# Kernel optimization log

Hardware: AMD Instinct MI355X
Metric: run time of the kernel (lower is better)

## Reference

```python
import jax, jax.numpy as jnp
import numpy as np

N_FIELDS = 8
HIDDEN = 128
GEO = 15
APP = 32
N_PTS = 524288


def setup_inputs() -> dict:
    key = jax.random.key(0)
    ks = jax.random.split(key, 12)
    cin = 3 + GEO + APP  # color-net input dim = 50
    s = 0.05
    return {
        "positions": jax.random.normal(ks[0], (N_PTS, 3), jnp.float32),
        "directions": jax.random.normal(ks[1], (N_PTS, 3), jnp.float32),
        "appearance_embedding": jax.random.normal(ks[2], (N_PTS, APP), jnp.float32),
        "centroids": jax.random.normal(ks[3], (N_FIELDS, 3), jnp.float32),
        "Wd1": jax.random.normal(ks[4], (N_FIELDS, 3, HIDDEN), jnp.float32) * s,
        "bd1": jnp.zeros((N_FIELDS, HIDDEN), jnp.float32),
        "Wd2": jax.random.normal(ks[5], (N_FIELDS, HIDDEN, 1 + GEO), jnp.float32) * s,
        "bd2": jnp.zeros((N_FIELDS, 1 + GEO), jnp.float32),
        "Wc1": jax.random.normal(ks[6], (N_FIELDS, cin, HIDDEN), jnp.float32) * s,
        "bc1": jnp.zeros((N_FIELDS, HIDDEN), jnp.float32),
        "Wc2": jax.random.normal(ks[7], (N_FIELDS, HIDDEN, 3), jnp.float32) * s,
        "bc2": jnp.zeros((N_FIELDS, 3), jnp.float32),
    }


def reference(positions, directions, appearance_embedding, centroids,
              Wd1, bd1, Wd2, bd2, Wc1, bc1, Wc2, bc2):
    # --- routing: nearest centroid (cdist + argmin); squared dist has same argmin ---
    d2 = jnp.sum((positions[:, None, :] - centroids[None, :, :]) ** 2, axis=-1)  # [N, F]
    assign = jnp.argmin(d2, axis=1)  # [N] int

    n = positions.shape[0]
    density = jnp.zeros((n, 1), positions.dtype)
    rgb = jnp.zeros((n, 3), positions.dtype)

    # dispatch/combine: masked dense evaluation per field (small fixed field count)
    for i in range(N_FIELDS):
        mask = (assign == i)[:, None]
        # field.density_fn: 2-layer MLP, trunc_exp density activation
        h = jax.nn.relu(positions @ Wd1[i] + bd1[i])          # [N, H]
        dout = h @ Wd2[i] + bd2[i]                            # [N, 1+GEO]
        dens_i = jnp.exp(dout[:, :1])                         # trunc_exp
        geo_i = dout[:, 1:]                                   # density embedding
        # field.get_outputs: color head on (dirs, geo_feat, appearance)
        cin = jnp.concatenate([directions, geo_i, appearance_embedding], axis=-1)
        hc = jax.nn.relu(cin @ Wc1[i] + bc1[i])               # [N, H]
        rgb_i = jax.nn.sigmoid(hc @ Wc2[i] + bc2[i])          # [N, 3]
        density = jnp.where(mask, dens_i, density)
        rgb = jnp.where(mask, rgb_i, rgb)

    # outputs concatenated: [density | rgb] -> [N, 4]
    return jnp.concatenate([density, rgb], axis=-1)
```

## Files before the change

kernel.cpp:

```cpp
#include <hip/hip_runtime.h>
#include <math.h>

#define NF 8
#define HID 128
#define TILE 768
#define NIT 12

typedef _Float16 f16;
typedef _Float16 h2 __attribute__((ext_vector_type(2)));
typedef _Float16 f16x8 __attribute__((ext_vector_type(8)));
typedef float f32x4 __attribute__((ext_vector_type(4)));
typedef unsigned int u32;
typedef u32 u32x2 __attribute__((ext_vector_type(2)));
typedef u32 u32x4 __attribute__((ext_vector_type(4)));

__device__ __forceinline__ u32 pk(float a, float b) {
    return __builtin_bit_cast(u32, __builtin_amdgcn_cvt_pkrtz(a, b));
}
__device__ __forceinline__ float dot2a(u32 a, u32 b, float c) {
    return __builtin_amdgcn_fdot2(__builtin_bit_cast(h2, a),
                                  __builtin_bit_cast(h2, b), c, false);
}
__device__ __forceinline__ void lfence() {
    asm volatile("s_waitcnt lgkmcnt(0)" ::: "memory");
}


__device__ __forceinline__ int assign_field(float px, float py, float pz,
                                            const float* __restrict__ cen) {
    int best = 0;
    float bd = 3.4e38f;
#pragma unroll
    for (int k = 0; k < NF; ++k) {
        float dx = px - cen[k * 3 + 0];
        float dy = py - cen[k * 3 + 1];
        float dz = pz - cen[k * 3 + 2];
        float d = fmaf(dx, dx, fmaf(dy, dy, dz * dz));
        if (d < bd) { bd = d; best = k; }
    }
    return best;
}

__global__ void k_count(const float* __restrict__ pos, const float* __restrict__ cen,
                        int n, int* __restrict__ blockcnt) {
    __shared__ int lc[NF];
    int tid = threadIdx.x;
    if (tid < NF) lc[tid] = 0;
    __syncthreads();
    int i4 = blockIdx.x * blockDim.x + tid;
    int base = i4 * 4;
    if (base + 3 < n) {
        const float4* p4 = (const float4*)pos;
        float4 a = p4[i4 * 3 + 0];
        float4 b = p4[i4 * 3 + 1];
        float4 c = p4[i4 * 3 + 2];
        atomicAdd(&lc[assign_field(a.x, a.y, a.z, cen)], 1);
        atomicAdd(&lc[assign_field(a.w, b.x, b.y, cen)], 1);
        atomicAdd(&lc[assign_field(b.z, b.w, c.x, cen)], 1);
        atomicAdd(&lc[assign_field(c.y, c.z, c.w, cen)], 1);
    } else {
        for (int i = base; i < n; ++i)
            atomicAdd(&lc[assign_field(pos[3 * i], pos[3 * i + 1], pos[3 * i + 2], cen)], 1);
    }
    __syncthreads();
    if (tid < NF) blockcnt[blockIdx.x * NF + tid] = lc[tid];
}

__global__ void k_scatscan(const float* __restrict__ pos, const float* __restrict__ cen,
                           int n, int nb, int* __restrict__ ws) {
    const int tid = threadIdx.x;
    const int f = tid >> 6, lane = tid & 63;
    const int* c = ws + 32;
    int* perm = ws + 32 + nb * NF;
    __shared__ int totals[NF], pres[NF], starts[NF], cur[NF];

    int tot = 0, pre = 0;
    for (int b = lane; b < nb; b += 64) {
        int v = c[b * NF + f];
        tot += v;
        if (b < (int)blockIdx.x) pre += v;
    }
#pragma unroll
    for (int d = 1; d < 64; d <<= 1) {
        tot += __shfl_xor(tot, d, 64);
        pre += __shfl_xor(pre, d, 64);
    }
    if (lane == 0) { totals[f] = tot; pres[f] = pre; }
    __syncthreads();
    if (tid == 0) {
        int s = 0, tp = 0;
        for (int k = 0; k < NF; ++k) {
            starts[k] = s;
            if (blockIdx.x == 0) {
                ws[k] = totals[k];
                ws[8 + k] = s;
                ws[16 + k] = tp;
            }
            s += totals[k];
            tp += (totals[k] + TILE - 1) / TILE;
        }
        if (blockIdx.x == 0) ws[24] = tp;
    }
    __syncthreads();
    if (tid < NF) cur[tid] = starts[tid] + pres[tid];
    __syncthreads();

    int i4 = blockIdx.x * blockDim.x + tid;
    int base = i4 * 4;
    if (base + 3 < n) {
        const float4* p4 = (const float4*)pos;
        float4 a = p4[i4 * 3 + 0];
        float4 b = p4[i4 * 3 + 1];
        float4 cc = p4[i4 * 3 + 2];
        int f0 = assign_field(a.x, a.y, a.z, cen);
        int f1 = assign_field(a.w, b.x, b.y, cen);
        int f2 = assign_field(b.z, b.w, cc.x, cen);
        int f3 = assign_field(cc.y, cc.z, cc.w, cen);
        perm[atomicAdd(&cur[f0], 1)] = base;
        perm[atomicAdd(&cur[f1], 1)] = base + 1;
        perm[atomicAdd(&cur[f2], 1)] = base + 2;
        perm[atomicAdd(&cur[f3], 1)] = base + 3;
    } else {
        for (int i = base; i < n; ++i) {
            int ff = assign_field(pos[3 * i], pos[3 * i + 1], pos[3 * i + 2], cen);
            perm[atomicAdd(&cur[ff], 1)] = i;
        }
    }
}

#define LDPERM(IT)                                                            \
    ({                                                                        \
        int _plc = tstart + (IT) * 64 + w * 16 + pt;                          \
        if (_plc > cnt - 1) _plc = cnt - 1;                                   \
        perm[start + _plc];                                                   \
    })

#define GATHER(IT2, PX, PY, PZ, D0, D1, D2, A0, A1, A2, A3, GI)               \
    {                                                                         \
        const int _nb = tstart + (IT2) * 64 + w * 16;                         \
        if ((IT2) < NIT && _nb < cnt) {                                       \
            if (quad == 0) {                                                  \
                PX = positions[(GI) * 3 + 0];                                 \
                PY = positions[(GI) * 3 + 1];                                 \
                PZ = positions[(GI) * 3 + 2];                                 \
            } else if (quad == 3) {                                           \
                D0 = directions[(GI) * 3 + 0];                                \
                D1 = directions[(GI) * 3 + 1];                                \
                D2 = directions[(GI) * 3 + 2];                                \
            } else {                                                          \
                const float4* _ap = (const float4*)(app + (GI) * 32) +        \
                                    (quad == 2 ? 4 : 0);                      \
                A0 = _ap[0]; A1 = _ap[1]; A2 = _ap[2]; A3 = _ap[3];           \
            }                                                                 \
        }                                                                     \
    }

#define STAGE(PX, PY, PZ, D0, D1, D2, A0, A1, A2, A3, CI)                     \
    {                                                                         \
        if (quad == 0) {                                                      \
            sIdx[w][pt] = (CI);                                               \
        } else if (quad == 3) {                                               \
            u32x2 _d; _d.x = pk(D0, D1); _d.y = pk(D2, 1.f);                  \
            *(u32x2*)&sCin[w][pt * 72] = _d;                                  \
        } else if (quad == 1) {                                               \
            u32x4 _v0, _v1;                                                   \
            _v0.x = pk(A0.x, A0.y); _v0.y = pk(A0.z, A0.w);                   \
            _v0.z = pk(A1.x, A1.y); _v0.w = pk(A1.z, A1.w);                   \
            _v1.x = pk(A2.x, A2.y); _v1.y = pk(A2.z, A2.w);                   \
            _v1.z = pk(A3.x, A3.y); _v1.w = pk(A3.z, A3.w);                   \
            *(u32x4*)&sCin[w][pt * 72 + 8] = _v0;                             \
            *(u32x4*)&sCin[w][pt * 72 + 16] = _v1;                            \
        } else {                                                              \
            u32x4 _v0, _v1;                                                   \
            _v0.x = pk(A0.x, A0.y); _v0.y = pk(A0.z, A0.w);                   \
            _v0.z = pk(A1.x, A1.y); _v0.w = pk(A1.z, A1.w);                   \
            _v1.x = pk(A2.x, A2.y); _v1.y = pk(A2.z, A2.w);                   \
            _v1.z = pk(A3.x, A3.y); _v1.w = pk(A3.z, A3.w);                   \
            *(u32x4*)&sCin[w][pt * 72 + 24] = _v0;                            \
            *(u32x4*)&sCin[w][pt * 72 + 32] = _v1;                           \
        }                                                                     \
    }

#define COMPUTE(CI, X01, X23)                                                 \
    {                                                                         \
        u32x4 _xv; _xv.x = (X01); _xv.y = (X23); _xv.z = 0u; _xv.w = 0u;      \
        const f16x8 _xb = __builtin_bit_cast(f16x8, _xv);                     \
        _Pragma("unroll")                                                     \
        for (int mt = 0; mt < 8; ++mt) {                                      \
            u32x4 _av; _av.x = wd1a0[mt]; _av.y = wd1a1[mt];                  \
            _av.z = 0u; _av.w = 0u;                                           \
            f16x8 _af = __builtin_bit_cast(f16x8, _av);                       \
            f32x4 _acc = {0.f, 0.f, 0.f, 0.f};                                \
            _acc = __builtin_amdgcn_mfma_f32_16x16x32_f16(_af, _xb, _acc, 0, 0, 0); \
            u32x2 _hw;                                                        \
            _hw.x = pk(fmaxf(_acc[0], 0.f), fmaxf(_acc[1], 0.f));             \
            _hw.y = pk(fmaxf(_acc[2], 0.f), fmaxf(_acc[3], 0.f));             \
            *(u32x2*)&sH[w][pt * 136 + 16 * mt + quad * 4] = _hw;             \
        }                                                                     \
        lfence();                                                             \
        f32x4 _dacc = {bd2v, bd2v, bd2v, bd2v};                               \
        _Pragma("unroll")                                                     \
        for (int s = 0; s < 4; ++s) {                                         \
            f16x8 _ha = __builtin_bit_cast(f16x8,                             \
                *(const u32x4*)&sH[w][pt * 136 + quad * 8 + 32 * s]);         \
            _dacc = __builtin_amdgcn_mfma_f32_16x16x32_f16(_ha, wd2b[s], _dacc, 0, 0, 0); \
        }                                                                     \
        if (pt == 0) {                                                        \
            int4 _si = *(const int4*)&sIdx[w][quad * 4];                      \
            out[_si.x * 4] = __expf(_dacc[0]);                                \
            out[_si.y * 4] = __expf(_dacc[1]);                                \
            out[_si.z * 4] = __expf(_dacc[2]);                                \
            out[_si.w * 4] = __expf(_dacc[3]);                                \
        } else {                                                              \
            _Pragma("unroll")                                                 \
            for (int r = 0; r < 4; ++r)                                       \
                sCin[w][(quad * 4 + r) * 72 + 40 + (pt - 1)] = (f16)_dacc[r]; \
        }                                                                     \
        lfence();                                                             \
        const f16x8 _cb0 = __builtin_bit_cast(f16x8,                          \
            *(const u32x4*)&sCin[w][pt * 72 + quad * 8]);                     \
        const f16x8 _cb1 = __builtin_bit_cast(f16x8,                          \
            *(const u32x4*)&sCin[w][pt * 72 + quad * 8 + 32]);                \
        float _r0 = 0.f, _r1 = 0.f, _r2 = 0.f;                                \
        _Pragma("unroll")                                                     \
        for (int mt = 0; mt < 8; ++mt) {                                      \
            f16x8 _wa0 = __builtin_bit_cast(f16x8,                            \
                *(const u32x4*)&sWc1t[(16 * mt + pt) * 72 + quad * 8]);       \
            f16x8 _wa1 = __builtin_bit_cast(f16x8,                            \
                *(const u32x4*)&sWc1t[(16 * mt + pt) * 72 + quad * 8 + 32]);  \
            f32x4 _cacc = {0.f, 0.f, 0.f, 0.f};                               \
            _cacc = __builtin_amdgcn_mfma_f32_16x16x32_f16(_wa0, _cb0, _cacc, 0, 0, 0); \
            _cacc = __builtin_amdgcn_mfma_f32_16x16x32_f16(_wa1, _cb1, _cacc, 0, 0, 0); \
            u32 _h01 = pk(fmaxf(_cacc[0], 0.f), fmaxf(_cacc[1], 0.f));        \
            u32 _h23 = pk(fmaxf(_cacc[2], 0.f), fmaxf(_cacc[3], 0.f));        \
            u32x4 _w01 = *(const u32x4*)&sWc2p[(8 * mt + 2 * quad) * 4];      \
            u32x4 _w23 = *(const u32x4*)&sWc2p[(8 * mt + 2 * quad + 1) * 4];  \
            _r0 = dot2a(_h01, _w01.x, _r0); _r0 = dot2a(_h23, _w23.x, _r0);   \
            _r1 = dot2a(_h01, _w01.y, _r1); _r1 = dot2a(_h23, _w23.y, _r1);   \
            _r2 = dot2a(_h01, _w01.z, _r2); _r2 = dot2a(_h23, _w23.z, _r2);   \
        }                                                                     \
        _r0 += __shfl_xor(_r0, 16, 64); _r0 += __shfl_xor(_r0, 32, 64);       \
        _r1 += __shfl_xor(_r1, 16, 64); _r1 += __shfl_xor(_r1, 32, 64);       \
        _r2 += __shfl_xor(_r2, 16, 64); _r2 += __shfl_xor(_r2, 32, 64);       \
        if (quad == 0) {                                                      \
            float _s0 = 1.f / (1.f + __expf(-(_r0 + c20)));                   \
            float _s1 = 1.f / (1.f + __expf(-(_r1 + c21)));                   \
            float _s2 = 1.f / (1.f + __expf(-(_r2 + c22)));                   \
            out[(CI) * 4 + 1] = _s0;                                          \
            *(float2*)&out[(CI) * 4 + 2] = make_float2(_s1, _s2);             \
        }                                                                     \
    }

#define HALF(IT, PX, PY, PZ, D0, D1, D2, A0, A1, A2, A3, IDX, NIDX)           \
    {                                                                         \
        lfence();      \
        STAGE(PX, PY, PZ, D0, D1, D2, A0, A1, A2, A3, IDX);                   \
        const u32 _x01 = (quad == 0) ? pk(PX, PY) : 0u;                       \
        const u32 _x23 = (quad == 0) ? pk(PZ, 1.f) : 0u;                      \
        const int _ci = IDX;                                                  \
        GATHER((IT) + 2, PX, PY, PZ, D0, D1, D2, A0, A1, A2, A3, NIDX);       \
        IDX = NIDX;                                                           \
        if ((IT) + 4 < NIT) NIDX = LDPERM((IT) + 4);                          \
        lfence();                   \
        COMPUTE(_ci, _x01, _x23);                                             \
    }

__global__ __launch_bounds__(256, 3) void k_main(
    const float* __restrict__ positions, const float* __restrict__ directions,
    const float* __restrict__ app,
    const float* __restrict__ Wd1, const float* __restrict__ bd1,
    const float* __restrict__ Wd2, const float* __restrict__ bd2,
    const float* __restrict__ Wc1, const float* __restrict__ bc1,
    const float* __restrict__ Wc2, const float* __restrict__ bc2,
    const int* __restrict__ ws, int nb, float* __restrict__ out) {
    const int b = blockIdx.x;
    if (b >= ws[24]) return;
    int f = 0;
#pragma unroll
    for (int k = 1; k < NF; ++k) if (b >= ws[16 + k]) f = k;
    const int tile = b - ws[16 + f];
    const int cnt = ws[f];
    const int start = ws[8 + f];
    const int* perm = ws + 32 + nb * NF;
    const int tid = threadIdx.x;
    const int w = tid >> 6, lane = tid & 63;
    const int pt = lane & 15, quad = lane >> 4;

    __shared__ __align__(16) f16 sWc1t[HID * 72];
    __shared__ __align__(16) u32 sWc2p[64 * 4];
    __shared__ __align__(16) int sIdx[4][16];
    __shared__ __align__(16) f16 sCin[4][16 * 72];
    __shared__ __align__(16) f16 sH[4][16 * 136];

    if (tid < HID) {
        int h = tid;
        f16* row = &sWc1t[h * 72];
        const float* Wf = Wc1 + f * 50 * HID;
        row[0] = (f16)Wf[0 * HID + h];
        row[1] = (f16)Wf[1 * HID + h];
        row[2] = (f16)Wf[2 * HID + h];
        row[3] = (f16)bc1[f * HID + h];
        row[4] = 0; row[5] = 0; row[6] = 0; row[7] = 0;
        for (int a = 0; a < 32; ++a) row[8 + a] = (f16)Wf[(18 + a) * HID + h];
        for (int g = 0; g < 15; ++g) row[40 + g] = (f16)Wf[(3 + g) * HID + h];
        for (int z = 55; z < 72; ++z) row[z] = 0;
    }
    if (tid < 64) {
        int hp = tid;
        const float* W2 = Wc2 + f * HID * 3;
        sWc2p[hp * 4 + 0] = pk(W2[(2 * hp) * 3 + 0], W2[(2 * hp + 1) * 3 + 0]);
        sWc2p[hp * 4 + 1] = pk(W2[(2 * hp) * 3 + 1], W2[(2 * hp + 1) * 3 + 1]);
        sWc2p[hp * 4 + 2] = pk(W2[(2 * hp) * 3 + 2], W2[(2 * hp + 1) * 3 + 2]);
        sWc2p[hp * 4 + 3] = 0;
    }
    if (lane < 16) {
        f16* row = &sCin[w][pt * 72];
        u32x2 z2; z2.x = 0; z2.y = 0;
        *(u32x2*)&row[4] = z2;
        row[55] = 0;
        u32x4 z4; z4.x = 0; z4.y = 0; z4.z = 0; z4.w = 0;
        *(u32x4*)&row[56] = z4;
    }

    u32 wd1a0[8], wd1a1[8];
    if (quad == 0) {
        const float* W1 = Wd1 + f * 3 * HID;
        const float* B1 = bd1 + f * HID;
#pragma unroll
        for (int mt = 0; mt < 8; ++mt) {
            int m = 16 * mt + pt;
            wd1a0[mt] = pk(W1[m], W1[HID + m]);
            wd1a1[mt] = pk(W1[2 * HID + m], B1[m]);
        }
    } else {
#pragma unroll
        for (int mt = 0; mt < 8; ++mt) { wd1a0[mt] = 0; wd1a1[mt] = 0; }
    }
    f16x8 wd2b[4];
    {
        const float* W2d = Wd2 + f * HID * 16;
#pragma unroll
        for (int s = 0; s < 4; ++s) {
            u32x4 v;
#pragma unroll
            for (int jp = 0; jp < 4; ++jp) {
                int k = quad * 8 + 32 * s + 2 * jp;
                v[jp] = pk(W2d[k * 16 + pt], W2d[(k + 1) * 16 + pt]);
            }
            wd2b[s] = __builtin_bit_cast(f16x8, v);
        }
    }
    const float bd2v = bd2[f * 16 + pt];
    const float c20 = bc2[f * 3 + 0], c21 = bc2[f * 3 + 1], c22 = bc2[f * 3 + 2];
    __syncthreads();

    const int tstart = tile * TILE;

    float pxa, pya, pza, d0a, d1a, d2a;
    float4 a0a, a1a, a2a, a3a;
    float pxb, pyb, pzb, d0b, d1b, d2b;
    float4 a0b, a1b, a2b, a3b;

    int idxA = LDPERM(0);
    int idxB = LDPERM(1);
    GATHER(0, pxa, pya, pza, d0a, d1a, d2a, a0a, a1a, a2a, a3a, idxA);
    GATHER(1, pxb, pyb, pzb, d0b, d1b, d2b, a0b, a1b, a2b, a3b, idxB);
    int nidxA = LDPERM(2);
    int nidxB = LDPERM(3);

#pragma unroll 1
    for (int it = 0; it < NIT; it += 2) {
        if (tstart + it * 64 + w * 16 >= cnt) break;
        HALF(it, pxa, pya, pza, d0a, d1a, d2a, a0a, a1a, a2a, a3a, idxA, nidxA);
        if (tstart + (it + 1) * 64 + w * 16 >= cnt) break;
        HALF(it + 1, pxb, pyb, pzb, d0b, d1b, d2b, a0b, a1b, a2b, a3b, idxB, nidxB);
    }
}

extern "C" void kernel_launch(void* const* d_in, const int* in_sizes, int n_in,
                              void* d_out, int out_size, void* d_ws, size_t ws_size,
                              hipStream_t stream) {
    const float* positions = (const float*)d_in[0];
    const float* directions = (const float*)d_in[1];
    const float* app = (const float*)d_in[2];
    const float* centroids = (const float*)d_in[3];
    const float* Wd1 = (const float*)d_in[4];
    const float* bd1 = (const float*)d_in[5];
    const float* Wd2 = (const float*)d_in[6];
    const float* bd2 = (const float*)d_in[7];
    const float* Wc1 = (const float*)d_in[8];
    const float* bc1 = (const float*)d_in[9];
    const float* Wc2 = (const float*)d_in[10];
    const float* bc2 = (const float*)d_in[11];
    float* out = (float*)d_out;
    int* wsi = (int*)d_ws;
    const int n = in_sizes[0] / 3;
    const int nb = (n + 2047) / 2048;
    const int max_tiles = (n + TILE - 1) / TILE + NF;

    k_count<<<nb, 512, 0, stream>>>(positions, centroids, n, wsi + 32);
    k_scatscan<<<nb, 512, 0, stream>>>(positions, centroids, n, nb, wsi);
    k_main<<<max_tiles, 256, 0, stream>>>(positions, directions, app, Wd1, bd1, Wd2,
                                          bd2, Wc1, bc1, Wc2, bc2, wsi, nb, out);
}
```

Baseline: 63.64 us.

## Halve hidden-layer LDS buffer, shrink tile, and raise occupancy to four blocks

The density MLP's hidden layer is now computed in two 64-wide halves, each written to a smaller shared buffer and consumed by the second-layer MFMAs before the next half is produced, cutting per-wave LDS. Tile size drops from 12 to 9 iterations per block, with an odd-tail iteration added, and launch bounds request 4 blocks per CU instead of 3. One LDS wait between the gather and compute stages is removed. The aim is more resident waves and more blocks for latency hiding, at the cost of extra LDS fences per point group, possible register pressure, and a smaller amortisation of per-block weight loading.

Measured after the change: 87.69 us. 37.8% more time.

```diff
diff --git a/kernel.cpp b/kernel.cpp
--- a/kernel.cpp
+++ b/kernel.cpp
@@ -3,8 +3,8 @@
 
 #define NF 8
 #define HID 128
-#define TILE 768
-#define NIT 12
+#define TILE 576
+#define NIT 9
 
 typedef _Float16 f16;
 typedef _Float16 h2 __attribute__((ext_vector_type(2)));
@@ -186,7 +186,7 @@
         u32x4 _xv; _xv.x = (X01); _xv.y = (X23); _xv.z = 0u; _xv.w = 0u;      \
         const f16x8 _xb = __builtin_bit_cast(f16x8, _xv);                     \
         _Pragma("unroll")                                                     \
-        for (int mt = 0; mt < 8; ++mt) {                                      \
+        for (int mt = 0; mt < 4; ++mt) {                                      \
             u32x4 _av; _av.x = wd1a0[mt]; _av.y = wd1a1[mt];                  \
             _av.z = 0u; _av.w = 0u;                                           \
             f16x8 _af = __builtin_bit_cast(f16x8, _av);                       \
@@ -195,14 +195,34 @@
             u32x2 _hw;                                                        \
             _hw.x = pk(fmaxf(_acc[0], 0.f), fmaxf(_acc[1], 0.f));             \
             _hw.y = pk(fmaxf(_acc[2], 0.f), fmaxf(_acc[3], 0.f));             \
-            *(u32x2*)&sH[w][pt * 136 + 16 * mt + quad * 4] = _hw;             \
+            *(u32x2*)&sH[w][pt * 72 + 16 * mt + quad * 4] = _hw;              \
         }                                                                     \
         lfence();                                                             \
         f32x4 _dacc = {bd2v, bd2v, bd2v, bd2v};                               \
         _Pragma("unroll")                                                     \
-        for (int s = 0; s < 4; ++s) {                                         \
+        for (int s = 0; s < 2; ++s) {                                         \
             f16x8 _ha = __builtin_bit_cast(f16x8,                             \
-                *(const u32x4*)&sH[w][pt * 136 + quad * 8 + 32 * s]);         \
+                *(const u32x4*)&sH[w][pt * 72 + quad * 8 + 32 * s]);          \
+            _dacc = __builtin_amdgcn_mfma_f32_16x16x32_f16(_ha, wd2b[s], _dacc, 0, 0, 0); \
+        }                                                                     \
+        lfence();                                                             \
+        _Pragma("unroll")                                                     \
+        for (int mt = 4; mt < 8; ++mt) {                                      \
+            u32x4 _av; _av.x = wd1a0[mt]; _av.y = wd1a1[mt];                  \
+            _av.z = 0u; _av.w = 0u;                                           \
+            f16x8 _af = __builtin_bit_cast(f16x8, _av);                       \
+            f32x4 _acc = {0.f, 0.f, 0.f, 0.f};                                \
+            _acc = __builtin_amdgcn_mfma_f32_16x16x32_f16(_af, _xb, _acc, 0, 0, 0); \
+            u32x2 _hw;                                                        \
+            _hw.x = pk(fmaxf(_acc[0], 0.f), fmaxf(_acc[1], 0.f));             \
+            _hw.y = pk(fmaxf(_acc[2], 0.f), fmaxf(_acc[3], 0.f));             \
+            *(u32x2*)&sH[w][pt * 72 + 16 * (mt - 4) + quad * 4] = _hw;        \
+        }                                                                     \
+        lfence();                                                             \
+        _Pragma("unroll")                                                     \
+        for (int s = 2; s < 4; ++s) {                                         \
+            f16x8 _ha = __builtin_bit_cast(f16x8,                             \
+                *(const u32x4*)&sH[w][pt * 72 + quad * 8 + 32 * (s - 2)]);    \
             _dacc = __builtin_amdgcn_mfma_f32_16x16x32_f16(_ha, wd2b[s], _dacc, 0, 0, 0); \
         }                                                                     \
         if (pt == 0) {                                                        \
@@ -253,7 +273,7 @@
 
 #define HALF(IT, PX, PY, PZ, D0, D1, D2, A0, A1, A2, A3, IDX, NIDX)           \
     {                                                                         \
-        lfence();      \
+        lfence();   \
         STAGE(PX, PY, PZ, D0, D1, D2, A0, A1, A2, A3, IDX);                   \
         const u32 _x01 = (quad == 0) ? pk(PX, PY) : 0u;                       \
         const u32 _x23 = (quad == 0) ? pk(PZ, 1.f) : 0u;                      \
@@ -261,11 +281,10 @@
         GATHER((IT) + 2, PX, PY, PZ, D0, D1, D2, A0, A1, A2, A3, NIDX);       \
         IDX = NIDX;                                                           \
         if ((IT) + 4 < NIT) NIDX = LDPERM((IT) + 4);                          \
-        lfence();                   \
         COMPUTE(_ci, _x01, _x23);                                             \
     }
 
-__global__ __launch_bounds__(256, 3) void k_main(
+__global__ __launch_bounds__(256, 4) void k_main(
     const float* __restrict__ positions, const float* __restrict__ directions,
     const float* __restrict__ app,
     const float* __restrict__ Wd1, const float* __restrict__ bd1,
@@ -290,7 +309,7 @@
     __shared__ __align__(16) u32 sWc2p[64 * 4];
     __shared__ __align__(16) int sIdx[4][16];
     __shared__ __align__(16) f16 sCin[4][16 * 72];
-    __shared__ __align__(16) f16 sH[4][16 * 136];
+    __shared__ __align__(16) f16 sH[4][16 * 72];
 
     if (tid < HID) {
         int h = tid;
@@ -369,12 +388,18 @@
     int nidxB = LDPERM(3);
 
 #pragma unroll 1
-    for (int it = 0; it < NIT; it += 2) {
-        if (tstart + it * 64 + w * 16 >= cnt) break;
+    for (int it = 0; it + 1 < NIT; it += 2) {
+        if (tstart + it * 64 + w * 16 >= cnt) goto done;
         HALF(it, pxa, pya, pza, d0a, d1a, d2a, a0a, a1a, a2a, a3a, idxA, nidxA);
-        if (tstart + (it + 1) * 64 + w * 16 >= cnt) break;
+        if (tstart + (it + 1) * 64 + w * 16 >= cnt) goto done;
         HALF(it + 1, pxb, pyb, pzb, d0b, d1b, d2b, a0b, a1b, a2b, a3b, idxB, nidxB);
     }
+#if (NIT & 1)
+    if (tstart + (NIT - 1) * 64 + w * 16 < cnt) {
+        HALF(NIT - 1, pxa, pya, pza, d0a, d1a, d2a, a0a, a1a, a2a, a3a, idxA, nidxA);
+    }
+#endif
+done:;
 }
 
 extern "C" void kernel_launch(void* const* d_in, const int* in_sizes, int n_in,
```
